# Kernel optimization log

Hardware: AMD Instinct MI355X
Metric: run time of the kernel (lower is better)

The kernel has to match this reference:

```python
import jax, jax.numpy as jnp
import numpy as np

N = 524288
L, T, F = 24, 1 << 19, 2          # levels, hashmap size per level, features per level
BASE_RES, MAX_RES = 16, 2048
PRIMES = np.array([1, 2654435761, 805459861], dtype=np.uint32)
# per-level resolutions, geometric growth (instant-ngp)
_b = np.exp((np.log(MAX_RES) - np.log(BASE_RES)) / (L - 1))
RES = np.floor(BASE_RES * _b ** np.arange(L)).astype(np.float32)  # [L]
CORNERS = np.stack(np.meshgrid(*[[0, 1]] * 3, indexing='ij'), -1).reshape(8, 3)  # [8,3]


def hash_encode(points, table):
    # points in [-1,1]^3 (bb_sides=2.0) -> [0,1]^3
    x = (points + 1.0) * 0.5
    pos = x[:, None, :] * jnp.asarray(RES)[None, :, None]      # [N,L,3]
    pos0 = jnp.floor(pos)
    w = pos - pos0                                             # [N,L,3] trilinear weights
    c = pos0[:, :, None, :].astype(jnp.uint32) + jnp.asarray(CORNERS, jnp.uint32)[None, None]  # [N,L,8,3]
    p = jnp.asarray(PRIMES)
    idx = ((c[..., 0] * p[0]) ^ (c[..., 1] * p[1]) ^ (c[..., 2] * p[2])) & jnp.uint32(T - 1)   # [N,L,8]
    feats = table[jnp.arange(L)[None, :, None], idx]           # [N,L,8,F]
    cb = jnp.asarray(CORNERS, jnp.float32)[None, None]         # [1,1,8,3]
    wts = jnp.prod(cb * w[:, :, None, :] + (1.0 - cb) * (1.0 - w[:, :, None, :]), axis=-1)  # [N,L,8]
    out = jnp.sum(feats * wts[..., None], axis=2)              # [N,L,F]
    return out.reshape(points.shape[0], L * F)                 # [N,48]


def sh3_encode(d):
    # real spherical harmonics, degree 3 -> 9 coefficients
    x, y, z = d[:, 0], d[:, 1], d[:, 2]
    return jnp.stack([
        jnp.full_like(x, 0.28209479177387814),
        -0.48860251190291987 * y,
        0.48860251190291987 * z,
        -0.48860251190291987 * x,
        1.0925484305920792 * x * y,
        -1.0925484305920792 * y * z,
        0.31539156525252005 * (3.0 * z * z - 1.0),
        -1.0925484305920792 * x * z,
        0.5462742152960396 * (x * x - y * y),
    ], axis=-1)                                                # [N,9]


def _gelu(x):
    return jax.nn.gelu(x, approximate=False)


def reference(samples_3d, samples_dirs, hash_table,
              fw0, fb0, fw1, fb1, fw2, fb2, fw3, fb3,
              rw0, rb0, rw1, rb1, rw2, rb2, iter_nr):
    enc = hash_encode(samples_3d, hash_table)                  # [N,48]
    dirs_enc = jax.lax.stop_gradient(sh3_encode(samples_dirs)) # no-grad dir encoding
    # mlp_feat_and_density: 48->64->64->64->65, GELU hidden, last linear
    h = _gelu(enc @ fw0 + fb0)
    h = _gelu(h @ fw1 + fb1)
    h = _gelu(h @ fw2 + fb2)
    fad = h @ fw3 + fb3                                        # [N,65]
    density = jax.nn.softplus(fad[:, 0:1])                     # [N,1]
    feat_rgb = _gelu(fad[:, 1:65])                             # [N,64]
    x = jnp.concatenate([feat_rgb, dirs_enc], axis=1)          # [N,73]
    # mlp_rgb: 73->64->64->3, GELU hidden, last linear
    h = _gelu(x @ rw0 + rb0)
    h = _gelu(h @ rw1 + rb1)
    rgb = jax.nn.sigmoid(h @ rw2 + rb2)                        # [N,3]
    return rgb, density


def setup_inputs():
    key = jax.random.key(0)
    ks = jax.random.split(key, 24)
    pts = jax.random.uniform(ks[0], (N, 3), minval=-1.0, maxval=1.0)
    d = jax.random.normal(ks[1], (N, 3))
    d = d / jnp.linalg.norm(d, axis=-1, keepdims=True)
    table = jax.random.uniform(ks[2], (L, T, F), minval=-1e-4, maxval=1e-4)

    def lin(k, fi, fo):
        k1, k2 = jax.random.split(k)
        s = 1.0 / np.sqrt(fi)
        return (jax.random.uniform(k1, (fi, fo), minval=-s, maxval=s),
                jax.random.uniform(k2, (fo,), minval=-s, maxval=s))

    inp = {"samples_3d": pts, "samples_dirs": d, "hash_table": table}
    i = 3
    for j, (fi, fo) in enumerate([(48, 64), (64, 64), (64, 64), (64, 65)]):
        w, b = lin(ks[i], fi, fo); inp[f"fw{j}"] = w; inp[f"fb{j}"] = b; i += 1
    for j, (fi, fo) in enumerate([(73, 64), (64, 64), (64, 3)]):
        w, b = lin(ks[i], fi, fo); inp[f"rw{j}"] = w; inp[f"rb{j}"] = b; i += 1
    inp["iter_nr"] = 0
    return inp
```

## Files before the change

kernel.cpp:

```cpp
#include <hip/hip_runtime.h>
#include <math.h>

#define LVL 24
#define TMASK ((1u << 19) - 1u)

typedef short short8 __attribute__((ext_vector_type(8)));
typedef float floatx4 __attribute__((ext_vector_type(4)));

struct ResParams { float r[LVL]; };

__device__ __forceinline__ float bf2f(unsigned short b) {
  union { unsigned u; float f; } t; t.u = ((unsigned)b) << 16; return t.f;
}
__device__ __forceinline__ unsigned short f2bf(float f) {
  union { float f; unsigned u; } t; t.f = f;
  unsigned u = t.u;
  u += 0x7FFFu + ((u >> 16) & 1u);
  return (unsigned short)(u >> 16);
}
__device__ __forceinline__ float geluf(float x) {
  float a = fabsf(x) * 0.7071067811865476f;
  float t = __builtin_amdgcn_rcpf(fmaf(0.3275911f, a, 1.0f));
  float p = fmaf(t, 1.061405429f, -1.453152027f);
  p = fmaf(t, p, 1.421413741f);
  p = fmaf(t, p, -0.284496736f);
  p = fmaf(t, p, 0.254829592f);
  float er = 1.0f - p * t * __expf(-a * a);
  return 0.5f * x * (1.0f + copysignf(er, x));
}
__device__ __forceinline__ floatx4 mfma16(short8 a, short8 b, floatx4 c) {
  return __builtin_amdgcn_mfma_f32_16x16x32_bf16(a, b, c, 0, 0, 0);
}

#define L0_W 0
#define L1_W 4096
#define L2_W 8192
#define L3_W 12288
#define L4_W 17408
#define L5_W 23552
#define L6_W 27648
#define WIMG_SHORTS 28672
#define L0_F 0
#define L1_F 512
#define L2_F 1024
#define L3_F 1536
#define L4_F 2176
#define L5_F 2944
#define L6_F 3456

__device__ void prepF(const float* w, short* dst, int K, int NOUT, int KCH, int CBS) {
  int total = KCH * CBS * 64 * 8;
  for (int i = threadIdx.x; i < total; i += 256) {
    int j = i & 7;
    int lane = (i >> 3) & 63;
    int cbc = i >> 9;
    int cb = cbc % CBS;
    int c  = cbc / CBS;
    int n = cb * 16 + (lane & 15);
    int k = c * 32 + (lane >> 4) * 8 + j;
    short v = 0;
    if (k < K && n < NOUT) v = (short)f2bf(w[k * NOUT + n]);
    dst[i] = v;
  }
}
__global__ __launch_bounds__(256) void prep_weights(
    const float* __restrict__ fw0, const float* __restrict__ fb0,
    const float* __restrict__ fw1, const float* __restrict__ fb1,
    const float* __restrict__ fw2, const float* __restrict__ fb2,
    const float* __restrict__ fw3, const float* __restrict__ fb3,
    const float* __restrict__ rw0, const float* __restrict__ rb0,
    const float* __restrict__ rw1, const float* __restrict__ rb1,
    const float* __restrict__ rw2, const float* __restrict__ rb2,
    short* __restrict__ Wimg, float* __restrict__ Bimg)
{
  int b = blockIdx.x, tid = threadIdx.x;
  switch (b) {
    case 0: prepF(fw0, Wimg + L0_W, 48, 64, 2, 4); break;
    case 1: prepF(fw1, Wimg + L1_W, 64, 64, 2, 4); break;
    case 2: prepF(fw2, Wimg + L2_W, 64, 64, 2, 4); break;
    case 3: prepF(fw3, Wimg + L3_W, 64, 65, 2, 5); break;
    case 4: prepF(rw0, Wimg + L4_W, 73, 64, 3, 4); break;
    case 5: prepF(rw1, Wimg + L5_W, 64, 64, 2, 4); break;
    case 6: prepF(rw2, Wimg + L6_W, 64,  3, 2, 1); break;
    case 7:
      if (tid < 64) {
        Bimg[tid]       = fb0[tid];
        Bimg[64 + tid]  = fb1[tid];
        Bimg[128 + tid] = fb2[tid];
        Bimg[272 + tid] = rb0[tid];
        Bimg[336 + tid] = rb1[tid];
      }
      if (tid < 80) Bimg[192 + tid] = (tid < 65) ? fb3[tid] : 0.0f;
      if (tid < 16) Bimg[400 + tid] = (tid < 3) ? rb2[tid] : 0.0f;
      break;
  }
}

__global__ __launch_bounds__(256) void tbl_pack(
    const float* __restrict__ t, unsigned* __restrict__ q, int nent)
{
  int g = blockIdx.x * 256 + threadIdx.x;
  int stride = gridDim.x * 256;
  for (int e = g; e < nent; e += stride) {
    float2 v = *(const float2*)(t + (size_t)2 * e);
    q[e] = (unsigned)f2bf(v.x) | ((unsigned)f2bf(v.y) << 16);
  }
}

template<bool PACKED>
__global__ __launch_bounds__(256) void hash_encode_k(
    const float* __restrict__ pts, const float* __restrict__ tbl,
    const unsigned* __restrict__ tblq, unsigned* __restrict__ enc2,
    int N, ResParams rp)
{
  int bid = blockIdx.x;
  int l   = bid >> 11;
  int p   = ((bid & 2047) << 8) + threadIdx.x;
  float res = rp.r[l];

  float x = (pts[p * 3 + 0] + 1.0f) * 0.5f * res;
  float y = (pts[p * 3 + 1] + 1.0f) * 0.5f * res;
  float z = (pts[p * 3 + 2] + 1.0f) * 0.5f * res;
  float fx = floorf(x), fy = floorf(y), fz = floorf(z);
  float w0 = x - fx, w1 = y - fy, w2 = z - fz;
  unsigned c0 = (unsigned)fx, c1 = (unsigned)fy, c2 = (unsigned)fz;
  unsigned hy0 = c1 * 2654435761u, hy1 = hy0 + 2654435761u;
  unsigned hz0 = c2 * 805459861u,  hz1 = hz0 + 805459861u;
  bool ceven = ((c0 & 1u) == 0u);

  const unsigned* tq = PACKED ? (tblq + ((size_t)l << 19)) : nullptr;
  const float*    tf = PACKED ? nullptr : (tbl + ((size_t)l << 20));

  float f0 = 0.f, f1 = 0.f;
  #pragma unroll
  for (int yz = 0; yz < 4; ++yz) {
    unsigned hyz = ((yz & 2) ? hy1 : hy0) ^ ((yz & 1) ? hz1 : hz0);
    float wyz = ((yz & 2) ? w1 : 1.f - w1) * ((yz & 1) ? w2 : 1.f - w2);
    unsigned h0 = (c0 ^ hyz) & TMASK;
    unsigned h1 = ((c0 + 1u) ^ hyz) & TMASK;
    float e00, e01, e10, e11;
    if constexpr (PACKED) {
      unsigned v0, v1;
      if (ceven) {
        uint2 v = *(const uint2*)(tq + (h0 & ~1u));
        v0 = (h0 & 1u) ? v.y : v.x;
        v1 = (h0 & 1u) ? v.x : v.y;
      } else {
        v0 = tq[h0];
        v1 = tq[h1];
      }
      e00 = bf2f((unsigned short)(v0 & 0xffffu)); e01 = bf2f((unsigned short)(v0 >> 16));
      e10 = bf2f((unsigned short)(v1 & 0xffffu)); e11 = bf2f((unsigned short)(v1 >> 16));
    } else {
      if (ceven) {
        float4 v = *(const float4*)(tf + 2u * (h0 & ~1u));
        if (h0 & 1u) { e00 = v.z; e01 = v.w; e10 = v.x; e11 = v.y; }
        else         { e00 = v.x; e01 = v.y; e10 = v.z; e11 = v.w; }
      } else {
        float2 a = *(const float2*)(tf + 2u * h0);
        float2 b = *(const float2*)(tf + 2u * h1);
        e00 = a.x; e01 = a.y; e10 = b.x; e11 = b.y;
      }
    }
    float wa = (1.f - w0) * wyz, wb = w0 * wyz;
    f0 += wa * e00 + wb * e10;
    f1 += wa * e01 + wb * e11;
  }
  enc2[l * N + p] = (unsigned)f2bf(f0) | ((unsigned)f2bf(f1) << 16);
}

template<int KCH, int CBS>
__device__ __forceinline__ void run_layer_g(const short* At, const short8* Wf,
                                            int lane, int m, int quad, floatx4* acc) {
  #pragma unroll
  for (int cb = 0; cb < CBS; ++cb) acc[cb] = (floatx4){0.f, 0.f, 0.f, 0.f};
  #pragma unroll
  for (int c = 0; c < KCH; ++c) {
    short8 a = *(const short8*)(At + m * 104 + c * 32 + quad * 8);
    #pragma unroll
    for (int cb = 0; cb < CBS; ++cb) {
      short8 b = Wf[(c * CBS + cb) * 64 + lane];
      acc[cb] = mfma16(a, b, acc[cb]);
    }
  }
}

__global__ __launch_bounds__(256, 4) void mlp_g(
    const float* __restrict__ dirs,
    const unsigned* __restrict__ enc2,
    const short* __restrict__ Wimg, const float* __restrict__ Bimg,
    float* __restrict__ outp, int Nrows)
{
  __shared__ __align__(16) short Atile[4 * 16 * 104];
  __shared__ __align__(16) float Blds[416];

  const int tid  = threadIdx.x;
  const int wave = tid >> 6;
  const int lane = tid & 63;
  const int m    = lane & 15;
  const int quad = lane >> 4;
  const int row0 = blockIdx.x * 64 + wave * 16;
  short* At = Atile + wave * (16 * 104);
  const short8* Wf = (const short8*)Wimg;

  if (tid < 104) ((float4*)Blds)[tid] = ((const float4*)Bimg)[tid];

  if (lane < 16) {
    int row = row0 + lane;
    float dx = dirs[row * 3 + 0];
    float dy = dirs[row * 3 + 1];
    float dz = dirs[row * 3 + 2];
    short8 z8 = {0, 0, 0, 0, 0, 0, 0, 0};
    short8 s07;
    s07[0] = (short)f2bf(0.28209479177387814f);
    s07[1] = (short)f2bf(-0.48860251190291987f * dy);
    s07[2] = (short)f2bf(0.48860251190291987f * dz);
    s07[3] = (short)f2bf(-0.48860251190291987f * dx);
    s07[4] = (short)f2bf(1.0925484305920792f * dx * dy);
    s07[5] = (short)f2bf(-1.0925484305920792f * dy * dz);
    s07[6] = (short)f2bf(0.31539156525252005f * (3.0f * dz * dz - 1.0f));
    s07[7] = (short)f2bf(-1.0925484305920792f * dx * dz);
    short8 s8v = {0, 0, 0, 0, 0, 0, 0, 0};
    s8v[0] = (short)f2bf(0.5462742152960396f * (dx * dx - dy * dy));
    short* rb = At + lane * 104;
    *(short8*)(rb + 48) = z8;
    *(short8*)(rb + 56) = z8;
    *(short8*)(rb + 64) = s07;
    *(short8*)(rb + 72) = s8v;
    *(short8*)(rb + 80) = z8;
    *(short8*)(rb + 88) = z8;
    *(short8*)(rb + 96) = z8;
  }

  for (int i = lane; i < 16 * LVL; i += 64) {
    int l = i >> 4;
    int r = i & 15;
    unsigned v = enc2[l * Nrows + row0 + r];
    *(unsigned*)(At + r * 104 + 2 * l) = v;
  }

  __syncthreads();

  floatx4 acc[5];

  run_layer_g<2, 4>(At, Wf + L0_F, lane, m, quad, acc);
  #pragma unroll
  for (int cb = 0; cb < 4; ++cb) {
    float bc = Blds[0 + cb * 16 + m];
    #pragma unroll
    for (int r = 0; r < 4; ++r) {
      float v = geluf(acc[cb][r] + bc);
      At[(quad * 4 + r) * 104 + cb * 16 + m] = (short)f2bf(v);
    }
  }
  run_layer_g<2, 4>(At, Wf + L1_F, lane, m, quad, acc);
  #pragma unroll
  for (int cb = 0; cb < 4; ++cb) {
    float bc = Blds[64 + cb * 16 + m];
    #pragma unroll
    for (int r = 0; r < 4; ++r) {
      float v = geluf(acc[cb][r] + bc);
      At[(quad * 4 + r) * 104 + cb * 16 + m] = (short)f2bf(v);
    }
  }
  run_layer_g<2, 4>(At, Wf + L2_F, lane, m, quad, acc);
  #pragma unroll
  for (int cb = 0; cb < 4; ++cb) {
    float bc = Blds[128 + cb * 16 + m];
    #pragma unroll
    for (int r = 0; r < 4; ++r) {
      float v = geluf(acc[cb][r] + bc);
      At[(quad * 4 + r) * 104 + cb * 16 + m] = (short)f2bf(v);
    }
  }
  run_layer_g<2, 5>(At, Wf + L3_F, lane, m, quad, acc);
  #pragma unroll
  for (int cb = 0; cb < 5; ++cb) {
    int col = cb * 16 + m;
    float bc = Blds[192 + col];
    #pragma unroll
    for (int r = 0; r < 4; ++r) {
      float v = acc[cb][r] + bc;
      int row = quad * 4 + r;
      if (col == 0) {
        float d = (v > 15.f) ? v : __logf(1.0f + __expf(v));
        outp[3 * Nrows + row0 + row] = d;
      } else if (col <= 64) {
        At[row * 104 + (col - 1)] = (short)f2bf(geluf(v));
      }
    }
  }
  run_layer_g<3, 4>(At, Wf + L4_F, lane, m, quad, acc);
  #pragma unroll
  for (int cb = 0; cb < 4; ++cb) {
    float bc = Blds[272 + cb * 16 + m];
    #pragma unroll
    for (int r = 0; r < 4; ++r) {
      float v = geluf(acc[cb][r] + bc);
      At[(quad * 4 + r) * 104 + cb * 16 + m] = (short)f2bf(v);
    }
  }
  run_layer_g<2, 4>(At, Wf + L5_F, lane, m, quad, acc);
  #pragma unroll
  for (int cb = 0; cb < 4; ++cb) {
    float bc = Blds[336 + cb * 16 + m];
    #pragma unroll
    for (int r = 0; r < 4; ++r) {
      float v = geluf(acc[cb][r] + bc);
      At[(quad * 4 + r) * 104 + cb * 16 + m] = (short)f2bf(v);
    }
  }
  run_layer_g<2, 1>(At, Wf + L6_F, lane, m, quad, acc);
  {
    float bc = Blds[400 + m];
    #pragma unroll
    for (int r = 0; r < 4; ++r) {
      float v = acc[0][r] + bc;
      float s = __builtin_amdgcn_rcpf(1.0f + __expf(-v));
      if (m < 3) outp[(row0 + quad * 4 + r) * 3 + m] = s;
    }
  }
}

#define W0_OFF 0
#define W1_OFF 4608
#define W2_OFF 9216
#define W3_OFF 13824
#define R0_OFF 0
#define R1_OFF 6656
#define R2_OFF 11264

template<int K, int NOUT, int NROWS, int STRIDE>
__device__ void stageW(const float* w, short* dst, int tid) {
  for (int i = tid; i < NROWS * STRIDE; i += 256) {
    int n = i / STRIDE;
    int k = i - n * STRIDE;
    short v = 0;
    if (n < NOUT && k < K) v = (short)f2bf(w[k * NOUT + n]);
    dst[i] = v;
  }
}
template<int NOUT, int NPAD>
__device__ void stageB(const float* b, float* dst, int tid) {
  for (int i = tid; i < NPAD; i += 256) dst[i] = (i < NOUT) ? b[i] : 0.0f;
}
template<int KCH, int CBS, int WSTRIDE>
__device__ __forceinline__ void run_layer(const short* At, const short* Wb,
                                          int m, int quad, floatx4* acc) {
  #pragma unroll
  for (int cb = 0; cb < CBS; ++cb) acc[cb] = (floatx4){0.f, 0.f, 0.f, 0.f};
  #pragma unroll
  for (int c = 0; c < KCH; ++c) {
    short8 a = *(const short8*)(At + m * 104 + c * 32 + quad * 8);
    #pragma unroll
    for (int cb = 0; cb < CBS; ++cb) {
      short8 b = *(const short8*)(Wb + (cb * 16 + m) * WSTRIDE + c * 32 + quad * 8);
      acc[cb] = mfma16(a, b, acc[cb]);
    }
  }
}

__global__ __launch_bounds__(256, 2) void nerf_fused(
    const float* __restrict__ pts,
    const float* __restrict__ dirs,
    const float* __restrict__ tbl,
    const float* __restrict__ fw0, const float* __restrict__ fb0,
    const float* __restrict__ fw1, const float* __restrict__ fb1,
    const float* __restrict__ fw2, const float* __restrict__ fb2,
    const float* __restrict__ fw3, const float* __restrict__ fb3,
    const float* __restrict__ rw0, const float* __restrict__ rb0,
    const float* __restrict__ rw1, const float* __restrict__ rb1,
    const float* __restrict__ rw2, const float* __restrict__ rb2,
    float* __restrict__ outp, int Nrows, ResParams rp)
{
  __shared__ __align__(16) short Wlds[19584];
  __shared__ __align__(16) float Blds[272];
  __shared__ __align__(16) short Atile[4 * 16 * 104];

  const int tid  = threadIdx.x;
  const int wave = tid >> 6;
  const int lane = tid & 63;
  const int m    = lane & 15;
  const int quad = lane >> 4;
  const int row0 = blockIdx.x * 64 + wave * 16;
  short* At = Atile + wave * (16 * 104);

  stageW<48, 64, 64, 72>(fw0, Wlds + W0_OFF, tid);
  stageW<64, 64, 64, 72>(fw1, Wlds + W1_OFF, tid);
  stageW<64, 64, 64, 72>(fw2, Wlds + W2_OFF, tid);
  stageW<64, 65, 80, 72>(fw3, Wlds + W3_OFF, tid);
  stageB<64, 64>(fb0, Blds + 0,   tid);
  stageB<64, 64>(fb1, Blds + 64,  tid);
  stageB<64, 64>(fb2, Blds + 128, tid);
  stageB<65, 80>(fb3, Blds + 192, tid);

  if (lane < 16) {
    int row = row0 + lane;
    float dx = dirs[row * 3 + 0];
    float dy = dirs[row * 3 + 1];
    float dz = dirs[row * 3 + 2];
    short8 z8 = {0, 0, 0, 0, 0, 0, 0, 0};
    short8 s07;
    s07[0] = (short)f2bf(0.28209479177387814f);
    s07[1] = (short)f2bf(-0.48860251190291987f * dy);
    s07[2] = (short)f2bf(0.48860251190291987f * dz);
    s07[3] = (short)f2bf(-0.48860251190291987f * dx);
    s07[4] = (short)f2bf(1.0925484305920792f * dx * dy);
    s07[5] = (short)f2bf(-1.0925484305920792f * dy * dz);
    s07[6] = (short)f2bf(0.31539156525252005f * (3.0f * dz * dz - 1.0f));
    s07[7] = (short)f2bf(-1.0925484305920792f * dx * dz);
    short8 s8v = {0, 0, 0, 0, 0, 0, 0, 0};
    s8v[0] = (short)f2bf(0.5462742152960396f * (dx * dx - dy * dy));
    short* rb = At + lane * 104;
    *(short8*)(rb + 48) = z8;
    *(short8*)(rb + 56) = z8;
    *(short8*)(rb + 64) = s07;
    *(short8*)(rb + 72) = s8v;
    *(short8*)(rb + 80) = z8;
    *(short8*)(rb + 88) = z8;
    *(short8*)(rb + 96) = z8;
  }

  for (int t = lane; t < 16 * LVL; t += 64) {
    int r = t / LVL;
    int l = t - r * LVL;
    int row = row0 + r;
    float res = rp.r[l];
    float x = (pts[row * 3 + 0] + 1.0f) * 0.5f * res;
    float y = (pts[row * 3 + 1] + 1.0f) * 0.5f * res;
    float z = (pts[row * 3 + 2] + 1.0f) * 0.5f * res;
    float fx = floorf(x), fy = floorf(y), fz = floorf(z);
    float w0 = x - fx, w1 = y - fy, w2 = z - fz;
    unsigned c0 = (unsigned)fx, c1 = (unsigned)fy, c2 = (unsigned)fz;
    unsigned ha0 = c0, hb0 = c0 + 1u;
    unsigned ha1 = c1 * 2654435761u, hb1 = ha1 + 2654435761u;
    unsigned ha2 = c2 * 805459861u,  hb2 = ha2 + 805459861u;
    const float* tb = tbl + ((size_t)l << 20);
    float f0 = 0.f, f1 = 0.f;
    #pragma unroll
    for (int i = 0; i < 8; ++i) {
      unsigned h = ((i & 4) ? hb0 : ha0) ^ ((i & 2) ? hb1 : ha1) ^ ((i & 1) ? hb2 : ha2);
      float wt = ((i & 4) ? w0 : 1.f - w0) * ((i & 2) ? w1 : 1.f - w1) * ((i & 1) ? w2 : 1.f - w2);
      float2 fv = *(const float2*)(tb + 2u * (h & TMASK));
      f0 += wt * fv.x;
      f1 += wt * fv.y;
    }
    unsigned pk = (unsigned)f2bf(f0) | ((unsigned)f2bf(f1) << 16);
    *(unsigned*)(At + r * 104 + 2 * l) = pk;
  }

  __syncthreads();

  floatx4 acc[5];

  run_layer<2, 4, 72>(At, Wlds + W0_OFF, m, quad, acc);
  #pragma unroll
  for (int cb = 0; cb < 4; ++cb) {
    float bc = Blds[0 + cb * 16 + m];
    #pragma unroll
    for (int r = 0; r < 4; ++r) {
      float v = geluf(acc[cb][r] + bc);
      At[(quad * 4 + r) * 104 + cb * 16 + m] = (short)f2bf(v);
    }
  }
  run_layer<2, 4, 72>(At, Wlds + W1_OFF, m, quad, acc);
  #pragma unroll
  for (int cb = 0; cb < 4; ++cb) {
    float bc = Blds[64 + cb * 16 + m];
    #pragma unroll
    for (int r = 0; r < 4; ++r) {
      float v = geluf(acc[cb][r] + bc);
      At[(quad * 4 + r) * 104 + cb * 16 + m] = (short)f2bf(v);
    }
  }
  run_layer<2, 4, 72>(At, Wlds + W2_OFF, m, quad, acc);
  #pragma unroll
  for (int cb = 0; cb < 4; ++cb) {
    float bc = Blds[128 + cb * 16 + m];
    #pragma unroll
    for (int r = 0; r < 4; ++r) {
      float v = geluf(acc[cb][r] + bc);
      At[(quad * 4 + r) * 104 + cb * 16 + m] = (short)f2bf(v);
    }
  }
  run_layer<2, 5, 72>(At, Wlds + W3_OFF, m, quad, acc);
  #pragma unroll
  for (int cb = 0; cb < 5; ++cb) {
    int col = cb * 16 + m;
    float bc = Blds[192 + col];
    #pragma unroll
    for (int r = 0; r < 4; ++r) {
      float v = acc[cb][r] + bc;
      int row = quad * 4 + r;
      if (col == 0) {
        float d = (v > 15.f) ? v : __logf(1.0f + __expf(v));
        outp[3 * Nrows + row0 + row] = d;
      } else if (col <= 64) {
        At[row * 104 + (col - 1)] = (short)f2bf(geluf(v));
      }
    }
  }

  __syncthreads();

  stageW<73, 64, 64, 104>(rw0, Wlds + R0_OFF, tid);
  stageW<64, 64, 64,  72>(rw1, Wlds + R1_OFF, tid);
  stageW<64,  3, 16,  72>(rw2, Wlds + R2_OFF, tid);
  stageB<64, 64>(rb0, Blds + 0,   tid);
  stageB<64, 64>(rb1, Blds + 64,  tid);
  stageB< 3, 16>(rb2, Blds + 128, tid);

  __syncthreads();

  run_layer<3, 4, 104>(At, Wlds + R0_OFF, m, quad, acc);
  #pragma unroll
  for (int cb = 0; cb < 4; ++cb) {
    float bc = Blds[0 + cb * 16 + m];
    #pragma unroll
    for (int r = 0; r < 4; ++r) {
      float v = geluf(acc[cb][r] + bc);
      At[(quad * 4 + r) * 104 + cb * 16 + m] = (short)f2bf(v);
    }
  }
  run_layer<2, 4, 72>(At, Wlds + R1_OFF, m, quad, acc);
  #pragma unroll
  for (int cb = 0; cb < 4; ++cb) {
    float bc = Blds[64 + cb * 16 + m];
    #pragma unroll
    for (int r = 0; r < 4; ++r) {
      float v = geluf(acc[cb][r] + bc);
      At[(quad * 4 + r) * 104 + cb * 16 + m] = (short)f2bf(v);
    }
  }
  run_layer<2, 1, 72>(At, Wlds + R2_OFF, m, quad, acc);
  {
    float bc = Blds[128 + m];
    #pragma unroll
    for (int r = 0; r < 4; ++r) {
      float v = acc[0][r] + bc;
      float s = __builtin_amdgcn_rcpf(1.0f + __expf(-v));
      if (m < 3) outp[(row0 + quad * 4 + r) * 3 + m] = s;
    }
  }
}

extern "C" void kernel_launch(void* const* d_in, const int* in_sizes, int n_in,
                              void* d_out, int out_size, void* d_ws, size_t ws_size,
                              hipStream_t stream) {
  ResParams rp;
  double b = exp((log(2048.0) - log(16.0)) / 23.0);
  for (int l = 0; l < LVL; ++l) rp.r[l] = (float)floor(16.0 * pow(b, (double)l));

  const float* pts  = (const float*)d_in[0];
  const float* dirs = (const float*)d_in[1];
  const float* tbl  = (const float*)d_in[2];
  float* outp = (float*)d_out;

  int n = in_sizes[0] / 3;
  int mlp_blocks = n / 64;
  int nent = LVL << 19;
  size_t enc_b = (size_t)LVL * (size_t)n * 4u;
  size_t img_reserve = 65536;
  size_t tbl_b = (size_t)nent * 4u;
  size_t full_need = enc_b + img_reserve + tbl_b;
  size_t mid_need  = enc_b + img_reserve;

  unsigned* enc2 = (unsigned*)d_ws;
  short* Wimg = (short*)((char*)d_ws + enc_b);
  float* Bimg = (float*)((char*)d_ws + enc_b + 57344);
  unsigned* tblq = (unsigned*)((char*)d_ws + enc_b + img_reserve);
  int enc_blocks = LVL * (n / 256);

  if (ws_size >= full_need) {
    prep_weights<<<8, 256, 0, stream>>>(
        (const float*)d_in[3],  (const float*)d_in[4],
        (const float*)d_in[5],  (const float*)d_in[6],
        (const float*)d_in[7],  (const float*)d_in[8],
        (const float*)d_in[9],  (const float*)d_in[10],
        (const float*)d_in[11], (const float*)d_in[12],
        (const float*)d_in[13], (const float*)d_in[14],
        (const float*)d_in[15], (const float*)d_in[16],
        Wimg, Bimg);
    tbl_pack<<<12288, 256, 0, stream>>>(tbl, tblq, nent);
    hash_encode_k<true><<<enc_blocks, 256, 0, stream>>>(pts, tbl, tblq, enc2, n, rp);
    mlp_g<<<mlp_blocks, 256, 0, stream>>>(dirs, enc2, Wimg, Bimg, outp, n);
  } else if (ws_size >= mid_need) {
    prep_weights<<<8, 256, 0, stream>>>(
        (const float*)d_in[3],  (const float*)d_in[4],
        (const float*)d_in[5],  (const float*)d_in[6],
        (const float*)d_in[7],  (const float*)d_in[8],
        (const float*)d_in[9],  (const float*)d_in[10],
        (const float*)d_in[11], (const float*)d_in[12],
        (const float*)d_in[13], (const float*)d_in[14],
        (const float*)d_in[15], (const float*)d_in[16],
        Wimg, Bimg);
    hash_encode_k<false><<<enc_blocks, 256, 0, stream>>>(pts, tbl, nullptr, enc2, n, rp);
    mlp_g<<<mlp_blocks, 256, 0, stream>>>(dirs, enc2, Wimg, Bimg, outp, n);
  } else {
    nerf_fused<<<mlp_blocks, 256, 0, stream>>>(
        pts, dirs, tbl,
        (const float*)d_in[3],  (const float*)d_in[4],
        (const float*)d_in[5],  (const float*)d_in[6],
        (const float*)d_in[7],  (const float*)d_in[8],
        (const float*)d_in[9],  (const float*)d_in[10],
        (const float*)d_in[11], (const float*)d_in[12],
        (const float*)d_in[13], (const float*)d_in[14],
        (const float*)d_in[15], (const float*)d_in[16],
        outp, n, rp);
  }
}
```

Measured before the change: 529.2 us.

## Merge table pack into prep kernel, stage points via LDS, 32-row MLP tiles

Result: no change. 526.8 us (-0.5%).

```diff
diff --git a/kernel.cpp b/kernel.cpp
--- a/kernel.cpp
+++ b/kernel.cpp
@@ -63,7 +63,7 @@
     dst[i] = v;
   }
 }
-__global__ __launch_bounds__(256) void prep_weights(
+__global__ __launch_bounds__(256) void prep_all(
     const float* __restrict__ fw0, const float* __restrict__ fb0,
     const float* __restrict__ fw1, const float* __restrict__ fb1,
     const float* __restrict__ fw2, const float* __restrict__ fb2,
@@ -71,9 +71,21 @@
     const float* __restrict__ rw0, const float* __restrict__ rb0,
     const float* __restrict__ rw1, const float* __restrict__ rb1,
     const float* __restrict__ rw2, const float* __restrict__ rb2,
-    short* __restrict__ Wimg, float* __restrict__ Bimg)
+    short* __restrict__ Wimg, float* __restrict__ Bimg,
+    const float* __restrict__ tbl, unsigned* __restrict__ tblq, int nent,
+    int pack_on)
 {
   int b = blockIdx.x, tid = threadIdx.x;
+  if (b >= 8) {
+    if (!pack_on) return;
+    int g = (b - 8) * 256 + tid;
+    int stride = (gridDim.x - 8) * 256;
+    for (int e = g; e < nent; e += stride) {
+      float2 v = *(const float2*)(tbl + (size_t)2 * e);
+      tblq[e] = (unsigned)f2bf(v.x) | ((unsigned)f2bf(v.y) << 16);
+    }
+    return;
+  }
   switch (b) {
     case 0: prepF(fw0, Wimg + L0_W, 48, 64, 2, 4); break;
     case 1: prepF(fw1, Wimg + L1_W, 64, 64, 2, 4); break;
@@ -96,31 +108,31 @@
   }
 }
 
-__global__ __launch_bounds__(256) void tbl_pack(
-    const float* __restrict__ t, unsigned* __restrict__ q, int nent)
-{
-  int g = blockIdx.x * 256 + threadIdx.x;
-  int stride = gridDim.x * 256;
-  for (int e = g; e < nent; e += stride) {
-    float2 v = *(const float2*)(t + (size_t)2 * e);
-    q[e] = (unsigned)f2bf(v.x) | ((unsigned)f2bf(v.y) << 16);
-  }
-}
-
 template<bool PACKED>
 __global__ __launch_bounds__(256) void hash_encode_k(
     const float* __restrict__ pts, const float* __restrict__ tbl,
     const unsigned* __restrict__ tblq, unsigned* __restrict__ enc2,
     int N, ResParams rp)
 {
-  int bid = blockIdx.x;
-  int l   = bid >> 11;
-  int p   = ((bid & 2047) << 8) + threadIdx.x;
+  __shared__ float pbuf[4][192];
+  int bid  = blockIdx.x;
+  int wave = threadIdx.x >> 6;
+  int lane = threadIdx.x & 63;
+  int l    = bid >> 11;
+  int p0   = ((bid & 2047) << 8) + wave * 64;
+  int p    = p0 + lane;
   float res = rp.r[l];
 
-  float x = (pts[p * 3 + 0] + 1.0f) * 0.5f * res;
-  float y = (pts[p * 3 + 1] + 1.0f) * 0.5f * res;
-  float z = (pts[p * 3 + 2] + 1.0f) * 0.5f * res;
+  {
+    const float* pf = pts + (size_t)p0 * 3;
+    pbuf[wave][lane]       = pf[lane];
+    pbuf[wave][64 + lane]  = pf[64 + lane];
+    pbuf[wave][128 + lane] = pf[128 + lane];
+  }
+  float x = (pbuf[wave][lane * 3 + 0] + 1.0f) * 0.5f * res;
+  float y = (pbuf[wave][lane * 3 + 1] + 1.0f) * 0.5f * res;
+  float z = (pbuf[wave][lane * 3 + 2] + 1.0f) * 0.5f * res;
+
   float fx = floorf(x), fy = floorf(y), fz = floorf(z);
   float w0 = x - fx, w1 = y - fy, w2 = z - fz;
   unsigned c0 = (unsigned)fx, c1 = (unsigned)fy, c2 = (unsigned)fz;
@@ -170,17 +182,23 @@
 }
 
 template<int KCH, int CBS>
-__device__ __forceinline__ void run_layer_g(const short* At, const short8* Wf,
-                                            int lane, int m, int quad, floatx4* acc) {
-  #pragma unroll
-  for (int cb = 0; cb < CBS; ++cb) acc[cb] = (floatx4){0.f, 0.f, 0.f, 0.f};
+__device__ __forceinline__ void run_layer32(const short* At, const short8* Wf,
+                                            int lane, int m, int quad,
+                                            floatx4* acc0, floatx4* acc1) {
+  #pragma unroll
+  for (int cb = 0; cb < CBS; ++cb) {
+    acc0[cb] = (floatx4){0.f, 0.f, 0.f, 0.f};
+    acc1[cb] = (floatx4){0.f, 0.f, 0.f, 0.f};
+  }
   #pragma unroll
   for (int c = 0; c < KCH; ++c) {
-    short8 a = *(const short8*)(At + m * 104 + c * 32 + quad * 8);
+    short8 a0 = *(const short8*)(At + m * 104 + c * 32 + quad * 8);
+    short8 a1 = *(const short8*)(At + (16 + m) * 104 + c * 32 + quad * 8);
     #pragma unroll
     for (int cb = 0; cb < CBS; ++cb) {
       short8 b = Wf[(c * CBS + cb) * 64 + lane];
-      acc[cb] = mfma16(a, b, acc[cb]);
+      acc0[cb] = mfma16(a0, b, acc0[cb]);
+      acc1[cb] = mfma16(a1, b, acc1[cb]);
     }
   }
 }
@@ -191,8 +209,198 @@
     const short* __restrict__ Wimg, const float* __restrict__ Bimg,
     float* __restrict__ outp, int Nrows)
 {
+  __shared__ __align__(16) short Atile[4 * 32 * 104];
+  __shared__ __align__(16) float Blds[416];
+
+  const int tid  = threadIdx.x;
+  const int wave = tid >> 6;
+  const int lane = tid & 63;
+  const int m    = lane & 15;
+  const int quad = lane >> 4;
+  const int row0 = blockIdx.x * 128 + wave * 32;
+  short* At = Atile + wave * (32 * 104);
+  const short8* Wf = (const short8*)Wimg;
+
+  if (tid < 104) ((float4*)Blds)[tid] = ((const float4*)Bimg)[tid];
+
+  if (lane < 32) {
+    int row = row0 + lane;
+    float dx = dirs[row * 3 + 0];
+    float dy = dirs[row * 3 + 1];
+    float dz = dirs[row * 3 + 2];
+    short8 z8 = {0, 0, 0, 0, 0, 0, 0, 0};
+    short8 s07;
+    s07[0] = (short)f2bf(0.28209479177387814f);
+    s07[1] = (short)f2bf(-0.48860251190291987f * dy);
+    s07[2] = (short)f2bf(0.48860251190291987f * dz);
+    s07[3] = (short)f2bf(-0.48860251190291987f * dx);
+    s07[4] = (short)f2bf(1.0925484305920792f * dx * dy);
+    s07[5] = (short)f2bf(-1.0925484305920792f * dy * dz);
+    s07[6] = (short)f2bf(0.31539156525252005f * (3.0f * dz * dz - 1.0f));
+    s07[7] = (short)f2bf(-1.0925484305920792f * dx * dz);
+    short8 s8v = {0, 0, 0, 0, 0, 0, 0, 0};
+    s8v[0] = (short)f2bf(0.5462742152960396f * (dx * dx - dy * dy));
+    short* rb = At + lane * 104;
+    *(short8*)(rb + 48) = z8;
+    *(short8*)(rb + 56) = z8;
+    *(short8*)(rb + 64) = s07;
+    *(short8*)(rb + 72) = s8v;
+    *(short8*)(rb + 80) = z8;
+    *(short8*)(rb + 88) = z8;
+    *(short8*)(rb + 96) = z8;
+  }
+
+  for (int i = lane; i < 32 * LVL; i += 64) {
+    int l = i >> 5;
+    int r = i & 31;
+    unsigned v = enc2[l * Nrows + row0 + r];
+    *(unsigned*)(At + r * 104 + 2 * l) = v;
+  }
+
+  __syncthreads();
+
+  floatx4 acc0[5], acc1[5];
+
+  run_layer32<2, 4>(At, Wf + L0_F, lane, m, quad, acc0, acc1);
+  #pragma unroll
+  for (int cb = 0; cb < 4; ++cb) {
+    float bc = Blds[0 + cb * 16 + m];
+    #pragma unroll
+    for (int r = 0; r < 4; ++r) {
+      At[(quad * 4 + r) * 104 + cb * 16 + m]      = (short)f2bf(geluf(acc0[cb][r] + bc));
+      At[(16 + quad * 4 + r) * 104 + cb * 16 + m] = (short)f2bf(geluf(acc1[cb][r] + bc));
+    }
+  }
+  run_layer32<2, 4>(At, Wf + L1_F, lane, m, quad, acc0, acc1);
+  #pragma unroll
+  for (int cb = 0; cb < 4; ++cb) {
+    float bc = Blds[64 + cb * 16 + m];
+    #pragma unroll
+    for (int r = 0; r < 4; ++r) {
+      At[(quad * 4 + r) * 104 + cb * 16 + m]      = (short)f2bf(geluf(acc0[cb][r] + bc));
+      At[(16 + quad * 4 + r) * 104 + cb * 16 + m] = (short)f2bf(geluf(acc1[cb][r] + bc));
+    }
+  }
+  run_layer32<2, 4>(At, Wf + L2_F, lane, m, quad, acc0, acc1);
+  #pragma unroll
+  for (int cb = 0; cb < 4; ++cb) {
+    float bc = Blds[128 + cb * 16 + m];
+    #pragma unroll
+    for (int r = 0; r < 4; ++r) {
+      At[(quad * 4 + r) * 104 + cb * 16 + m]      = (short)f2bf(geluf(acc0[cb][r] + bc));
+      At[(16 + quad * 4 + r) * 104 + cb * 16 + m] = (short)f2bf(geluf(acc1[cb][r] + bc));
+    }
+  }
+  run_layer32<2, 5>(At, Wf + L3_F, lane, m, quad, acc0, acc1);
+  #pragma unroll
+  for (int cb = 0; cb < 5; ++cb) {
+    int col = cb * 16 + m;
+    float bc = Blds[192 + col];
+    #pragma unroll
+    for (int r = 0; r < 4; ++r) {
+      #pragma unroll
+      for (int t = 0; t < 2; ++t) {
+        float v = (t ? acc1[cb][r] : acc0[cb][r]) + bc;
+        int row = t * 16 + quad * 4 + r;
+        if (col == 0) {
+          float d = (v > 15.f) ? v : __logf(1.0f + __expf(v));
+          outp[3 * Nrows + row0 + row] = d;
+        } else if (col <= 64) {
+          At[row * 104 + (col - 1)] = (short)f2bf(geluf(v));
+        }
+      }
+    }
+  }
+  run_layer32<3, 4>(At, Wf + L4_F, lane, m, quad, acc0, acc1);
+  #pragma unroll
+  for (int cb = 0; cb < 4; ++cb) {
+    float bc = Blds[272 + cb * 16 + m];
+    #pragma unroll
+    for (int r = 0; r < 4; ++r) {
+      At[(quad * 4 + r) * 104 + cb * 16 + m]      = (short)f2bf(geluf(acc0[cb][r] + bc));
+      At[(16 + quad * 4 + r) * 104 + cb * 16 + m] = (short)f2bf(geluf(acc1[cb][r] + bc));
+    }
+  }
+  run_layer32<2, 4>(At, Wf + L5_F, lane, m, quad, acc0, acc1);
+  #pragma unroll
+  for (int cb = 0; cb < 4; ++cb) {
+    float bc = Blds[336 + cb * 16 + m];
+    #pragma unroll
+    for (int r = 0; r < 4; ++r) {
+      At[(quad * 4 + r) * 104 + cb * 16 + m]      = (short)f2bf(geluf(acc0[cb][r] + bc));
+      At[(16 + quad * 4 + r) * 104 + cb * 16 + m] = (short)f2bf(geluf(acc1[cb][r] + bc));
+    }
+  }
+  run_layer32<2, 1>(At, Wf + L6_F, lane, m, quad, acc0, acc1);
+  {
+    float bc = Blds[400 + m];
+    #pragma unroll
+    for (int r = 0; r < 4; ++r) {
+      #pragma unroll
+      for (int t = 0; t < 2; ++t) {
+        float v = (t ? acc1[0][r] : acc0[0][r]) + bc;
+        float s = __builtin_amdgcn_rcpf(1.0f + __expf(-v));
+        int row = t * 16 + quad * 4 + r;
+        if (m < 3) outp[(row0 + row) * 3 + m] = s;
+      }
+    }
+  }
+}
+
+#define W0_OFF 0
+#define W1_OFF 4608
+#define W2_OFF 9216
+#define W3_OFF 13824
+#define R0_OFF 0
+#define R1_OFF 6656
+#define R2_OFF 11264
+
+template<int K, int NOUT, int NROWS, int STRIDE>
+__device__ void stageW(const float* w, short* dst, int tid) {
+  for (int i = tid; i < NROWS * STRIDE; i += 256) {
+    int n = i / STRIDE;
+    int k = i - n * STRIDE;
+    short v = 0;
+    if (n < NOUT && k < K) v = (short)f2bf(w[k * NOUT + n]);
+    dst[i] = v;
+  }
+}
+template<int NOUT, int NPAD>
+__device__ void stageB(const float* b, float* dst, int tid) {
+  for (int i = tid; i < NPAD; i += 256) dst[i] = (i < NOUT) ? b[i] : 0.0f;
+}
+template<int KCH, int CBS, int WSTRIDE>
+__device__ __forceinline__ void run_layer(const short* At, const short* Wb,
+                                          int m, int quad, floatx4* acc) {
+  #pragma unroll
+  for (int cb = 0; cb < CBS; ++cb) acc[cb] = (floatx4){0.f, 0.f, 0.f, 0.f};
+  #pragma unroll
+  for (int c = 0; c < KCH; ++c) {
+    short8 a = *(const short8*)(At + m * 104 + c * 32 + quad * 8);
+    #pragma unroll
+    for (int cb = 0; cb < CBS; ++cb) {
+      short8 b = *(const short8*)(Wb + (cb * 16 + m) * WSTRIDE + c * 32 + quad * 8);
+      acc[cb] = mfma16(a, b, acc[cb]);
+    }
+  }
+}
+
+__global__ __launch_bounds__(256, 2) void nerf_fused(
+    const float* __restrict__ pts,
+    const float* __restrict__ dirs,
+    const float* __restrict__ tbl,
+    const float* __restrict__ fw0, const float* __restrict__ fb0,
+    const float* __restrict__ fw1, const float* __restrict__ fb1,
+    const float* __restrict__ fw2, const float* __restrict__ fb2,
+    const float* __restrict__ fw3, const float* __restrict__ fb3,
+    const float* __restrict__ rw0, const float* __restrict__ rb0,
+    const float* __restrict__ rw1, const float* __restrict__ rb1,
+    const float* __restrict__ rw2, const float* __restrict__ rb2,
+    float* __restrict__ outp, int Nrows, ResParams rp)
+{
+  __shared__ __align__(16) short Wlds[19584];
+  __shared__ __align__(16) float Blds[272];
   __shared__ __align__(16) short Atile[4 * 16 * 104];
-  __shared__ __align__(16) float Blds[416];
 
   const int tid  = threadIdx.x;
   const int wave = tid >> 6;
@@ -201,9 +409,15 @@
   const int quad = lane >> 4;
   const int row0 = blockIdx.x * 64 + wave * 16;
   short* At = Atile + wave * (16 * 104);
-  const short8* Wf = (const short8*)Wimg;
-
-  if (tid < 104) ((float4*)Blds)[tid] = ((const float4*)Bimg)[tid];
+
+  stageW<48, 64, 64, 72>(fw0, Wlds + W0_OFF, tid);
+  stageW<64, 64, 64, 72>(fw1, Wlds + W1_OFF, tid);
+  stageW<64, 64, 64, 72>(fw2, Wlds + W2_OFF, tid);
+  stageW<64, 65, 80, 72>(fw3, Wlds + W3_OFF, tid);
+  stageB<64, 64>(fb0, Blds + 0,   tid);
+  stageB<64, 64>(fb1, Blds + 64,  tid);
+  stageB<64, 64>(fb2, Blds + 128, tid);
+  stageB<65, 80>(fb3, Blds + 192, tid);
 
   if (lane < 16) {
     int row = row0 + lane;
@@ -232,195 +446,6 @@
     *(short8*)(rb + 96) = z8;
   }
 
-  for (int i = lane; i < 16 * LVL; i += 64) {
-    int l = i >> 4;
-    int r = i & 15;
-    unsigned v = enc2[l * Nrows + row0 + r];
-    *(unsigned*)(At + r * 104 + 2 * l) = v;
-  }
-
-  __syncthreads();
-
-  floatx4 acc[5];
-
-  run_layer_g<2, 4>(At, Wf + L0_F, lane, m, quad, acc);
-  #pragma unroll
-  for (int cb = 0; cb < 4; ++cb) {
-    float bc = Blds[0 + cb * 16 + m];
-    #pragma unroll
-    for (int r = 0; r < 4; ++r) {
-      float v = geluf(acc[cb][r] + bc);
-      At[(quad * 4 + r) * 104 + cb * 16 + m] = (short)f2bf(v);
-    }
-  }
-  run_layer_g<2, 4>(At, Wf + L1_F, lane, m, quad, acc);
-  #pragma unroll
-  for (int cb = 0; cb < 4; ++cb) {
-    float bc = Blds[64 + cb * 16 + m];
-    #pragma unroll
-    for (int r = 0; r < 4; ++r) {
-      float v = geluf(acc[cb][r] + bc);
-      At[(quad * 4 + r) * 104 + cb * 16 + m] = (short)f2bf(v);
-    }
-  }
-  run_layer_g<2, 4>(At, Wf + L2_F, lane, m, quad, acc);
-  #pragma unroll
-  for (int cb = 0; cb < 4; ++cb) {
-    float bc = Blds[128 + cb * 16 + m];
-    #pragma unroll
-    for (int r = 0; r < 4; ++r) {
-      float v = geluf(acc[cb][r] + bc);
-      At[(quad * 4 + r) * 104 + cb * 16 + m] = (short)f2bf(v);
-    }
-  }
-  run_layer_g<2, 5>(At, Wf + L3_F, lane, m, quad, acc);
-  #pragma unroll
-  for (int cb = 0; cb < 5; ++cb) {
-    int col = cb * 16 + m;
-    float bc = Blds[192 + col];
-    #pragma unroll
-    for (int r = 0; r < 4; ++r) {
-      float v = acc[cb][r] + bc;
-      int row = quad * 4 + r;
-      if (col == 0) {
-        float d = (v > 15.f) ? v : __logf(1.0f + __expf(v));
-        outp[3 * Nrows + row0 + row] = d;
-      } else if (col <= 64) {
-        At[row * 104 + (col - 1)] = (short)f2bf(geluf(v));
-      }
-    }
-  }
-  run_layer_g<3, 4>(At, Wf + L4_F, lane, m, quad, acc);
-  #pragma unroll
-  for (int cb = 0; cb < 4; ++cb) {
-    float bc = Blds[272 + cb * 16 + m];
-    #pragma unroll
-    for (int r = 0; r < 4; ++r) {
-      float v = geluf(acc[cb][r] + bc);
-      At[(quad * 4 + r) * 104 + cb * 16 + m] = (short)f2bf(v);
-    }
-  }
-  run_layer_g<2, 4>(At, Wf + L5_F, lane, m, quad, acc);
-  #pragma unroll
-  for (int cb = 0; cb < 4; ++cb) {
-    float bc = Blds[336 + cb * 16 + m];
-    #pragma unroll
-    for (int r = 0; r < 4; ++r) {
-      float v = geluf(acc[cb][r] + bc);
-      At[(quad * 4 + r) * 104 + cb * 16 + m] = (short)f2bf(v);
-    }
-  }
-  run_layer_g<2, 1>(At, Wf + L6_F, lane, m, quad, acc);
-  {
-    float bc = Blds[400 + m];
-    #pragma unroll
-    for (int r = 0; r < 4; ++r) {
-      float v = acc[0][r] + bc;
-      float s = __builtin_amdgcn_rcpf(1.0f + __expf(-v));
-      if (m < 3) outp[(row0 + quad * 4 + r) * 3 + m] = s;
-    }
-  }
-}
-
-#define W0_OFF 0
-#define W1_OFF 4608
-#define W2_OFF 9216
-#define W3_OFF 13824
-#define R0_OFF 0
-#define R1_OFF 6656
-#define R2_OFF 11264
-
-template<int K, int NOUT, int NROWS, int STRIDE>
-__device__ void stageW(const float* w, short* dst, int tid) {
-  for (int i = tid; i < NROWS * STRIDE; i += 256) {
-    int n = i / STRIDE;
-    int k = i - n * STRIDE;
-    short v = 0;
-    if (n < NOUT && k < K) v = (short)f2bf(w[k * NOUT + n]);
-    dst[i] = v;
-  }
-}
-template<int NOUT, int NPAD>
-__device__ void stageB(const float* b, float* dst, int tid) {
-  for (int i = tid; i < NPAD; i += 256) dst[i] = (i < NOUT) ? b[i] : 0.0f;
-}
-template<int KCH, int CBS, int WSTRIDE>
-__device__ __forceinline__ void run_layer(const short* At, const short* Wb,
-                                          int m, int quad, floatx4* acc) {
-  #pragma unroll
-  for (int cb = 0; cb < CBS; ++cb) acc[cb] = (floatx4){0.f, 0.f, 0.f, 0.f};
-  #pragma unroll
-  for (int c = 0; c < KCH; ++c) {
-    short8 a = *(const short8*)(At + m * 104 + c * 32 + quad * 8);
-    #pragma unroll
-    for (int cb = 0; cb < CBS; ++cb) {
-      short8 b = *(const short8*)(Wb + (cb * 16 + m) * WSTRIDE + c * 32 + quad * 8);
-      acc[cb] = mfma16(a, b, acc[cb]);
-    }
-  }
-}
-
-__global__ __launch_bounds__(256, 2) void nerf_fused(
-    const float* __restrict__ pts,
-    const float* __restrict__ dirs,
-    const float* __restrict__ tbl,
-    const float* __restrict__ fw0, const float* __restrict__ fb0,
-    const float* __restrict__ fw1, const float* __restrict__ fb1,
-    const float* __restrict__ fw2, const float* __restrict__ fb2,
-    const float* __restrict__ fw3, const float* __restrict__ fb3,
-    const float* __restrict__ rw0, const float* __restrict__ rb0,
-    const float* __restrict__ rw1, const float* __restrict__ rb1,
-    const float* __restrict__ rw2, const float* __restrict__ rb2,
-    float* __restrict__ outp, int Nrows, ResParams rp)
-{
-  __shared__ __align__(16) short Wlds[19584];
-  __shared__ __align__(16) float Blds[272];
-  __shared__ __align__(16) short Atile[4 * 16 * 104];
-
-  const int tid  = threadIdx.x;
-  const int wave = tid >> 6;
-  const int lane = tid & 63;
-  const int m    = lane & 15;
-  const int quad = lane >> 4;
-  const int row0 = blockIdx.x * 64 + wave * 16;
-  short* At = Atile + wave * (16 * 104);
-
-  stageW<48, 64, 64, 72>(fw0, Wlds + W0_OFF, tid);
-  stageW<64, 64, 64, 72>(fw1, Wlds + W1_OFF, tid);
-  stageW<64, 64, 64, 72>(fw2, Wlds + W2_OFF, tid);
-  stageW<64, 65, 80, 72>(fw3, Wlds + W3_OFF, tid);
-  stageB<64, 64>(fb0, Blds + 0,   tid);
-  stageB<64, 64>(fb1, Blds + 64,  tid);
-  stageB<64, 64>(fb2, Blds + 128, tid);
-  stageB<65, 80>(fb3, Blds + 192, tid);
-
-  if (lane < 16) {
-    int row = row0 + lane;
-    float dx = dirs[row * 3 + 0];
-    float dy = dirs[row * 3 + 1];
-    float dz = dirs[row * 3 + 2];
-    short8 z8 = {0, 0, 0, 0, 0, 0, 0, 0};
-    short8 s07;
-    s07[0] = (short)f2bf(0.28209479177387814f);
-    s07[1] = (short)f2bf(-0.48860251190291987f * dy);
-    s07[2] = (short)f2bf(0.48860251190291987f * dz);
-    s07[3] = (short)f2bf(-0.48860251190291987f * dx);
-    s07[4] = (short)f2bf(1.0925484305920792f * dx * dy);
-    s07[5] = (short)f2bf(-1.0925484305920792f * dy * dz);
-    s07[6] = (short)f2bf(0.31539156525252005f * (3.0f * dz * dz - 1.0f));
-    s07[7] = (short)f2bf(-1.0925484305920792f * dx * dz);
-    short8 s8v = {0, 0, 0, 0, 0, 0, 0, 0};
-    s8v[0] = (short)f2bf(0.5462742152960396f * (dx * dx - dy * dy));
-    short* rb = At + lane * 104;
-    *(short8*)(rb + 48) = z8;
-    *(short8*)(rb + 56) = z8;
-    *(short8*)(rb + 64) = s07;
-    *(short8*)(rb + 72) = s8v;
-    *(short8*)(rb + 80) = z8;
-    *(short8*)(rb + 88) = z8;
-    *(short8*)(rb + 96) = z8;
-  }
-
   for (int t = lane; t < 16 * LVL; t += 64) {
     int r = t / LVL;
     int l = t - r * LVL;
@@ -557,7 +582,6 @@
   float* outp = (float*)d_out;
 
   int n = in_sizes[0] / 3;
-  int mlp_blocks = n / 64;
   int nent = LVL << 19;
   size_t enc_b = (size_t)LVL * (size_t)n * 4u;
   size_t img_reserve = 65536;
@@ -570,9 +594,10 @@
   float* Bimg = (float*)((char*)d_ws + enc_b + 57344);
   unsigned* tblq = (unsigned*)((char*)d_ws + enc_b + img_reserve);
   int enc_blocks = LVL * (n / 256);
+  int mlp_blocks = n / 128;
 
   if (ws_size >= full_need) {
-    prep_weights<<<8, 256, 0, stream>>>(
+    prep_all<<<8 + 12288, 256, 0, stream>>>(
         (const float*)d_in[3],  (const float*)d_in[4],
         (const float*)d_in[5],  (const float*)d_in[6],
         (const float*)d_in[7],  (const float*)d_in[8],
@@ -580,12 +605,11 @@
         (const float*)d_in[11], (const float*)d_in[12],
         (const float*)d_in[13], (const float*)d_in[14],
         (const float*)d_in[15], (const float*)d_in[16],
-        Wimg, Bimg);
-    tbl_pack<<<12288, 256, 0, stream>>>(tbl, tblq, nent);
+        Wimg, Bimg, tbl, tblq, nent, 1);
     hash_encode_k<true><<<enc_blocks, 256, 0, stream>>>(pts, tbl, tblq, enc2, n, rp);
     mlp_g<<<mlp_blocks, 256, 0, stream>>>(dirs, enc2, Wimg, Bimg, outp, n);
   } else if (ws_size >= mid_need) {
-    prep_weights<<<8, 256, 0, stream>>>(
+    prep_all<<<8, 256, 0, stream>>>(
         (const float*)d_in[3],  (const float*)d_in[4],
         (const float*)d_in[5],  (const float*)d_in[6],
         (const float*)d_in[7],  (const float*)d_in[8],
@@ -593,11 +617,11 @@
         (const float*)d_in[11], (const float*)d_in[12],
         (const float*)d_in[13], (const float*)d_in[14],
         (const float*)d_in[15], (const float*)d_in[16],
-        Wimg, Bimg);
+        Wimg, Bimg, tbl, nullptr, nent, 0);
     hash_encode_k<false><<<enc_blocks, 256, 0, stream>>>(pts, tbl, nullptr, enc2, n, rp);
     mlp_g<<<mlp_blocks, 256, 0, stream>>>(dirs, enc2, Wimg, Bimg, outp, n);
   } else {
-    nerf_fused<<<mlp_blocks, 256, 0, stream>>>(
+    nerf_fused<<<n / 64, 256, 0, stream>>>(
         pts, dirs, tbl,
         (const float*)d_in[3],  (const float*)d_in[4],
         (const float*)d_in[5],  (const float*)d_in[6],
```
